# Performance work log

Hardware: AMD Instinct MI355X
Metric: run time of the kernel (lower is better)

The kernel has to match this reference:

```python
import jax, jax.numpy as jnp
import numpy as np

BLOCK = 16
MAX_LEVEL = 4
D = 256
W_INSIDE = 16.0  # CrossEntropyLoss weight for class 0
W_OUTSIDE = 1.0  # weight for class 1


def _blocks(gt, bs):
    # gt: [D,D,D] int -> [nb^3, bs, bs, bs] blocks in (x,y,z) order
    nb = gt.shape[0] // bs
    b = gt.reshape(nb, bs, nb, bs, nb, bs)
    return jnp.transpose(b, (0, 2, 4, 1, 3, 5)).reshape(nb ** 3, bs, bs, bs)


def setup_inputs() -> dict:
    key = jax.random.key(0)
    k1, k2, k3 = jax.random.split(key, 3)
    gt_label = jax.random.randint(k1, (1, D, D, D), 0, 2, dtype=jnp.int32)
    preds_full = jax.random.normal(k2, (4096, 2, BLOCK, BLOCK, BLOCK), dtype=jnp.float32)
    preds_single = jax.random.uniform(k3, (585, 3), dtype=jnp.float32)
    return {"gt_label": gt_label, "preds_full": preds_full, "preds_single": preds_single}


def reference(gt_label, preds_full, preds_single):
    gt = gt_label[0]  # [D,D,D]

    # ---- level 0: weighted cross-entropy per dense block (loss_fulls / loss_full_single) ----
    tgt = _blocks(gt, BLOCK)                              # [4096,16,16,16]
    logp = jax.nn.log_softmax(preds_full, axis=1)         # [4096,2,16,16,16]
    nll = -jnp.take_along_axis(logp, tgt[:, None].astype(jnp.int32), axis=1)[:, 0]
    w = jnp.where(tgt == 0, W_INSIDE, W_OUTSIDE)
    # torch weighted-mean CE: sum(w*nll)/sum(w) per block, then summed over blocks
    loss0 = jnp.sum(jnp.sum(w * nll, axis=(1, 2, 3)) / jnp.sum(w, axis=(1, 2, 3)))

    # ---- levels 1..MAX_LEVEL: ret += log(pred[0, gt]) per block (loss_singles) ----
    total = loss0
    offset = 0
    for level in range(1, MAX_LEVEL + 1):
        bs = BLOCK * 2 ** level
        nb = D // bs
        n = nb ** 3
        blk = _blocks(gt, bs).reshape(n, -1)
        mx = blk.max(axis=1)
        mn = blk.min(axis=1)
        g = jnp.where(mx != mn, 2, mx)                    # MIXED=2 or pure label
        p = preds_single[offset:offset + n]               # [n,3]
        total = total + jnp.sum(jnp.log(jnp.take_along_axis(p, g[:, None], axis=1)))
        offset += n
    return total
```

## Files before the change

kernel.cpp:

```cpp
#include <hip/hip_runtime.h>


#define W_INSIDE 16.0f

__global__ __launch_bounds__(256) void level0_kernel(
    const int* __restrict__ gt,
    const float* __restrict__ preds,
    unsigned char* __restrict__ flags,
    float* __restrict__ out)
{
    const int n  = blockIdx.x;
    const int bi = n >> 8, bj = (n >> 4) & 15, bk = n & 15;
    const int gbase = (bi * 16) * 65536 + (bj * 16) * 256 + (bk * 16);
    const float* __restrict__ p0 = preds + (size_t)n * 8192;
    const float* __restrict__ p1 = p0 + 4096;
    const int t = threadIdx.x;

    float wnll = 0.0f, wsum = 0.0f;
    int mn = 1, mx = 0;

    #pragma unroll
    for (int i = 0; i < 4; ++i) {
        const int v4 = t + 256 * i;
        const int x  = v4 >> 6;
        const int y  = (v4 >> 2) & 15;
        const int z4 = (v4 & 3) * 4;
        const int4   g4 = *reinterpret_cast<const int4*>(gt + gbase + x * 65536 + y * 256 + z4);
        const float4 a  = *reinterpret_cast<const float4*>(p0 + 4 * v4);
        const float4 b  = *reinterpret_cast<const float4*>(p1 + 4 * v4);

        const int   gs[4] = {g4.x, g4.y, g4.z, g4.w};
        const float av[4] = {a.x, a.y, a.z, a.w};
        const float bv[4] = {b.x, b.y, b.z, b.w};
        #pragma unroll
        for (int j = 0; j < 4; ++j) {
            const int tg = gs[j];
            mn = min(mn, tg);
            mx = max(mx, tg);
            const float d   = tg ? (bv[j] - av[j]) : (av[j] - bv[j]);
            const float nll = fmaxf(-d, 0.0f) + __logf(1.0f + __expf(-fabsf(d)));
            const float w   = tg ? 1.0f : W_INSIDE;
            wnll += w * nll;
            wsum += w;
        }
    }

    #pragma unroll
    for (int off = 32; off > 0; off >>= 1) {
        wnll += __shfl_down(wnll, off, 64);
        wsum += __shfl_down(wsum, off, 64);
        mn = min(mn, __shfl_down(mn, off, 64));
        mx = max(mx, __shfl_down(mx, off, 64));
    }
    __shared__ float s_wnll[4], s_wsum[4];
    __shared__ int   s_mn[4], s_mx[4];
    const int wave = t >> 6;
    if ((t & 63) == 0) { s_wnll[wave] = wnll; s_wsum[wave] = wsum; s_mn[wave] = mn; s_mx[wave] = mx; }
    __syncthreads();
    if (t == 0) {
        float W = 0.0f, S = 0.0f; int MN = 1, MX = 0;
        #pragma unroll
        for (int w = 0; w < 4; ++w) {
            W += s_wnll[w]; S += s_wsum[w];
            MN = min(MN, s_mn[w]); MX = max(MX, s_mx[w]);
        }
        atomicAdd(out, W / S);
        flags[n] = (unsigned char)(MN | (MX << 1));
    }
}

__global__ __launch_bounds__(512) void levels_kernel(
    const unsigned char* __restrict__ flags,
    const float* __restrict__ ps,
    float* __restrict__ out)
{
    __shared__ unsigned char s1[512];
    __shared__ unsigned char s2[64];
    __shared__ unsigned char s3[8];
    const int t = threadIdx.x;
    float acc = 0.0f;

    {
        const int bi = t >> 6, bj = (t >> 3) & 7, bk = t & 7;
        int mn = 1, mx = 0;
        #pragma unroll
        for (int di = 0; di < 2; ++di)
        #pragma unroll
        for (int dj = 0; dj < 2; ++dj)
        #pragma unroll
        for (int dk = 0; dk < 2; ++dk) {
            const unsigned char c = flags[(2*bi+di)*256 + (2*bj+dj)*16 + (2*bk+dk)];
            mn &= (c & 1);
            mx |= ((c >> 1) & 1);
        }
        const int g = (mn == mx) ? mx : 2;
        acc += __logf(ps[(0 + t) * 3 + g]);
        s1[t] = (unsigned char)(mn | (mx << 1));
    }
    __syncthreads();

    if (t < 64) {
        const int bi = t >> 4, bj = (t >> 2) & 3, bk = t & 3;
        int mn = 1, mx = 0;
        #pragma unroll
        for (int di = 0; di < 2; ++di)
        #pragma unroll
        for (int dj = 0; dj < 2; ++dj)
        #pragma unroll
        for (int dk = 0; dk < 2; ++dk) {
            const unsigned char c = s1[(2*bi+di)*64 + (2*bj+dj)*8 + (2*bk+dk)];
            mn &= (c & 1);
            mx |= ((c >> 1) & 1);
        }
        const int g = (mn == mx) ? mx : 2;
        acc += __logf(ps[(512 + t) * 3 + g]);
        s2[t] = (unsigned char)(mn | (mx << 1));
    }
    __syncthreads();

    if (t < 8) {
        const int bi = t >> 2, bj = (t >> 1) & 1, bk = t & 1;
        int mn = 1, mx = 0;
        #pragma unroll
        for (int di = 0; di < 2; ++di)
        #pragma unroll
        for (int dj = 0; dj < 2; ++dj)
        #pragma unroll
        for (int dk = 0; dk < 2; ++dk) {
            const unsigned char c = s2[(2*bi+di)*16 + (2*bj+dj)*4 + (2*bk+dk)];
            mn &= (c & 1);
            mx |= ((c >> 1) & 1);
        }
        const int g = (mn == mx) ? mx : 2;
        acc += __logf(ps[(576 + t) * 3 + g]);
        s3[t] = (unsigned char)(mn | (mx << 1));
    }
    __syncthreads();

    if (t == 0) {
        int mn = 1, mx = 0;
        #pragma unroll
        for (int c8 = 0; c8 < 8; ++c8) {
            mn &= (s3[c8] & 1);
            mx |= ((s3[c8] >> 1) & 1);
        }
        const int g = (mn == mx) ? mx : 2;
        acc += __logf(ps[584 * 3 + g]);
    }

    #pragma unroll
    for (int off = 32; off > 0; off >>= 1)
        acc += __shfl_down(acc, off, 64);
    __shared__ float s_acc[8];
    const int wave = t >> 6;
    if ((t & 63) == 0) s_acc[wave] = acc;
    __syncthreads();
    if (t == 0) {
        float S = 0.0f;
        #pragma unroll
        for (int w = 0; w < 8; ++w) S += s_acc[w];
        atomicAdd(out, S);
    }
}

extern "C" void kernel_launch(void* const* d_in, const int* in_sizes, int n_in,
                              void* d_out, int out_size, void* d_ws, size_t ws_size,
                              hipStream_t stream) {
    const int*   gt    = (const int*)d_in[0];
    const float* preds = (const float*)d_in[1];
    const float* ps    = (const float*)d_in[2];
    float* out = (float*)d_out;
    unsigned char* flags = (unsigned char*)d_ws;

    hipMemsetAsync(d_out, 0, out_size * sizeof(float), stream);
    level0_kernel<<<4096, 256, 0, stream>>>(gt, preds, flags, out);
    levels_kernel<<<1, 512, 0, stream>>>(flags, ps, out);
}
```

Before: 249.1 us.

## Pre-pack labels into per-block bitmasks and drop atomics and memset

Adds a pass that streams the int32 label volume once and packs it into 16-bit masks laid out per 16^3 block, so the level-0 kernel reads a compact mask instead of strided int4 label loads. Level-0 now issues all prediction loads up front with nontemporal hints and writes per-block losses to a buffer instead of using atomics. The final single-block kernel sums those losses and writes the output directly, which removes the memset. The cost is an extra kernel launch and an extra round trip of the label data, though the mask it writes back is small.

New measurement: 229.5 us. -7.9%, faster.

```diff
diff --git a/kernel.cpp b/kernel.cpp
--- a/kernel.cpp
+++ b/kernel.cpp
@@ -3,73 +3,111 @@
 
 #define W_INSIDE 16.0f
 
-__global__ __launch_bounds__(256) void level0_kernel(
+typedef int   vint4   __attribute__((ext_vector_type(4)));
+typedef float vfloat4 __attribute__((ext_vector_type(4)));
+
+__global__ __launch_bounds__(256) void gt_pack_kernel(
     const int* __restrict__ gt,
+    unsigned short* __restrict__ mask)
+{
+    const int T = blockIdx.x * 256 + threadIdx.x;
+    const vint4* p = reinterpret_cast<const vint4*>(gt) + 4 * (size_t)T;
+    const vint4 q0 = __builtin_nontemporal_load(p + 0);
+    const vint4 q1 = __builtin_nontemporal_load(p + 1);
+    const vint4 q2 = __builtin_nontemporal_load(p + 2);
+    const vint4 q3 = __builtin_nontemporal_load(p + 3);
+
+    unsigned m = 0;
+    m |= (q0.x & 1)        | ((q0.y & 1) << 1)  | ((q0.z & 1) << 2)  | ((q0.w & 1) << 3);
+    m |= ((q1.x & 1) << 4) | ((q1.y & 1) << 5)  | ((q1.z & 1) << 6)  | ((q1.w & 1) << 7);
+    m |= ((q2.x & 1) << 8) | ((q2.y & 1) << 9)  | ((q2.z & 1) << 10) | ((q2.w & 1) << 11);
+    m |= ((q3.x & 1) << 12)| ((q3.y & 1) << 13) | ((q3.z & 1) << 14) | ((q3.w & 1) << 15);
+
+    const int x = T >> 12, y = (T >> 4) & 255, z16 = T & 15;
+    const int n = ((x >> 4) << 8) | ((y >> 4) << 4) | z16;
+    mask[n * 256 + (x & 15) * 16 + (y & 15)] = (unsigned short)m;
+}
+
+__global__ __launch_bounds__(256, 4) void level0_kernel(
     const float* __restrict__ preds,
-    unsigned char* __restrict__ flags,
-    float* __restrict__ out)
+    const unsigned short* __restrict__ mask,
+    float* __restrict__ loss,
+    unsigned char* __restrict__ flags)
 {
-    const int n  = blockIdx.x;
-    const int bi = n >> 8, bj = (n >> 4) & 15, bk = n & 15;
-    const int gbase = (bi * 16) * 65536 + (bj * 16) * 256 + (bk * 16);
-    const float* __restrict__ p0 = preds + (size_t)n * 8192;
-    const float* __restrict__ p1 = p0 + 4096;
+    const int n = blockIdx.x;
     const int t = threadIdx.x;
+    const vfloat4* __restrict__ p0 = reinterpret_cast<const vfloat4*>(preds + (size_t)n * 8192);
+    const vfloat4* __restrict__ p1 = p0 + 1024;
+
+    const vfloat4 a0 = __builtin_nontemporal_load(p0 + t);
+    const vfloat4 a1 = __builtin_nontemporal_load(p0 + t + 256);
+    const vfloat4 a2 = __builtin_nontemporal_load(p0 + t + 512);
+    const vfloat4 a3 = __builtin_nontemporal_load(p0 + t + 768);
+    const vfloat4 b0 = __builtin_nontemporal_load(p1 + t);
+    const vfloat4 b1 = __builtin_nontemporal_load(p1 + t + 256);
+    const vfloat4 b2 = __builtin_nontemporal_load(p1 + t + 512);
+    const vfloat4 b3 = __builtin_nontemporal_load(p1 + t + 768);
+    __builtin_amdgcn_sched_barrier(0);
+
+    __shared__ unsigned short smask[256];
+    if (t < 32)
+        reinterpret_cast<vint4*>(smask)[t] =
+            *(reinterpret_cast<const vint4*>(mask + (size_t)n * 256) + t);
+    __syncthreads();
 
     float wnll = 0.0f, wsum = 0.0f;
-    int mn = 1, mx = 0;
-
-    #pragma unroll
-    for (int i = 0; i < 4; ++i) {
-        const int v4 = t + 256 * i;
-        const int x  = v4 >> 6;
-        const int y  = (v4 >> 2) & 15;
-        const int z4 = (v4 & 3) * 4;
-        const int4   g4 = *reinterpret_cast<const int4*>(gt + gbase + x * 65536 + y * 256 + z4);
-        const float4 a  = *reinterpret_cast<const float4*>(p0 + 4 * v4);
-        const float4 b  = *reinterpret_cast<const float4*>(p1 + 4 * v4);
-
-        const int   gs[4] = {g4.x, g4.y, g4.z, g4.w};
-        const float av[4] = {a.x, a.y, a.z, a.w};
-        const float bv[4] = {b.x, b.y, b.z, b.w};
-        #pragma unroll
-        for (int j = 0; j < 4; ++j) {
-            const int tg = gs[j];
-            mn = min(mn, tg);
-            mx = max(mx, tg);
-            const float d   = tg ? (bv[j] - av[j]) : (av[j] - bv[j]);
-            const float nll = fmaxf(-d, 0.0f) + __logf(1.0f + __expf(-fabsf(d)));
-            const float w   = tg ? 1.0f : W_INSIDE;
-            wnll += w * nll;
-            wsum += w;
-        }
-    }
+    unsigned andb = 0xFu, orb = 0u;
+
+    #define DO4(V, A, B)                                                          \
+    {                                                                             \
+        const int x_ = (V) >> 6, y_ = ((V) >> 2) & 15, z4_ = (V) & 3;             \
+        const unsigned bits = ((unsigned)smask[x_ * 16 + y_] >> (z4_ * 4)) & 0xFu;\
+        andb &= bits; orb |= bits;                                                \
+        const float av[4] = {A.x, A.y, A.z, A.w};                                 \
+        const float bv[4] = {B.x, B.y, B.z, B.w};                                 \
+        _Pragma("unroll")                                                         \
+        for (int j = 0; j < 4; ++j) {                                             \
+            const int tg = (bits >> j) & 1;                                       \
+            const float d   = tg ? (bv[j] - av[j]) : (av[j] - bv[j]);             \
+            const float nll = fmaxf(-d, 0.0f) + __logf(1.0f + __expf(-fabsf(d))); \
+            wnll += tg ? nll : W_INSIDE * nll;                                    \
+            wsum += tg ? 1.0f : W_INSIDE;                                         \
+        }                                                                         \
+    }
+    DO4(t,       a0, b0)
+    DO4(t + 256, a1, b1)
+    DO4(t + 512, a2, b2)
+    DO4(t + 768, a3, b3)
+    #undef DO4
 
     #pragma unroll
     for (int off = 32; off > 0; off >>= 1) {
         wnll += __shfl_down(wnll, off, 64);
         wsum += __shfl_down(wsum, off, 64);
-        mn = min(mn, __shfl_down(mn, off, 64));
-        mx = max(mx, __shfl_down(mx, off, 64));
+        andb &= (unsigned)__shfl_down((int)andb, off, 64);
+        orb  |= (unsigned)__shfl_down((int)orb,  off, 64);
     }
     __shared__ float s_wnll[4], s_wsum[4];
-    __shared__ int   s_mn[4], s_mx[4];
+    __shared__ unsigned s_and[4], s_or[4];
     const int wave = t >> 6;
-    if ((t & 63) == 0) { s_wnll[wave] = wnll; s_wsum[wave] = wsum; s_mn[wave] = mn; s_mx[wave] = mx; }
+    if ((t & 63) == 0) { s_wnll[wave] = wnll; s_wsum[wave] = wsum; s_and[wave] = andb; s_or[wave] = orb; }
     __syncthreads();
     if (t == 0) {
-        float W = 0.0f, S = 0.0f; int MN = 1, MX = 0;
+        float W = 0.0f, S = 0.0f; unsigned A_ = 0xFu, O_ = 0u;
         #pragma unroll
         for (int w = 0; w < 4; ++w) {
             W += s_wnll[w]; S += s_wsum[w];
-            MN = min(MN, s_mn[w]); MX = max(MX, s_mx[w]);
-        }
-        atomicAdd(out, W / S);
-        flags[n] = (unsigned char)(MN | (MX << 1));
+            A_ &= s_and[w]; O_ |= s_or[w];
+        }
+        loss[n]  = W / S;
+        const int mn = (A_ == 0xFu) ? 1 : 0;
+        const int mx = O_ ? 1 : 0;
+        flags[n] = (unsigned char)(mn | (mx << 1));
     }
 }
 
 __global__ __launch_bounds__(512) void levels_kernel(
+    const float* __restrict__ loss,
     const unsigned char* __restrict__ flags,
     const float* __restrict__ ps,
     float* __restrict__ out)
@@ -81,6 +119,12 @@
     float acc = 0.0f;
 
     {
+        const vfloat4 l0 = *(reinterpret_cast<const vfloat4*>(loss) + 2 * t);
+        const vfloat4 l1 = *(reinterpret_cast<const vfloat4*>(loss) + 2 * t + 1);
+        acc += (l0.x + l0.y) + (l0.z + l0.w) + (l1.x + l1.y) + (l1.z + l1.w);
+    }
+
+    {
         const int bi = t >> 6, bj = (t >> 3) & 7, bk = t & 7;
         int mn = 1, mx = 0;
         #pragma unroll
@@ -159,7 +203,7 @@
         float S = 0.0f;
         #pragma unroll
         for (int w = 0; w < 8; ++w) S += s_acc[w];
-        atomicAdd(out, S);
+        out[0] = S;
     }
 }
 
@@ -170,9 +214,12 @@
     const float* preds = (const float*)d_in[1];
     const float* ps    = (const float*)d_in[2];
     float* out = (float*)d_out;
-    unsigned char* flags = (unsigned char*)d_ws;
-
-    hipMemsetAsync(d_out, 0, out_size * sizeof(float), stream);
-    level0_kernel<<<4096, 256, 0, stream>>>(gt, preds, flags, out);
-    levels_kernel<<<1, 512, 0, stream>>>(flags, ps, out);
-}
+
+    unsigned short* maskbuf = (unsigned short*)d_ws;
+    float*          loss    = (float*)((char*)d_ws + (1 << 21));
+    unsigned char*  flagbuf = (unsigned char*)d_ws + (1 << 21) + 16384;
+
+    gt_pack_kernel<<<4096, 256, 0, stream>>>(gt, maskbuf);
+    level0_kernel<<<4096, 256, 0, stream>>>(preds, maskbuf, loss, flagbuf);
+    levels_kernel<<<1, 512, 0, stream>>>(loss, flagbuf, ps, out);
+}
```

## Process four z-adjacent blocks per workgroup with double-buffered loads and packed labels

Applied to the files above, without the earlier changes.

Each workgroup now handles four consecutive z blocks (1024 workgroups instead of 4096). Labels are loaded once as fully coalesced 64-byte rows, packed into 4-bit nibbles in shared memory, and the prediction loads are double-buffered against the compute. Weight sums come from popcounts of the packed labels. Per-block losses go to a workspace buffer that the second kernel sums, which removes the memset and the global atomics. The changes add register pressure, shared-memory traffic and scheduling barriers, and use nontemporal loads.

Result: faster. 218.5 us (-12.3%).

```diff
diff --git a/kernel.cpp b/kernel.cpp
--- a/kernel.cpp
+++ b/kernel.cpp
@@ -3,73 +3,106 @@
 
 #define W_INSIDE 16.0f
 
-__global__ __launch_bounds__(256) void level0_kernel(
+typedef int   vint4   __attribute__((ext_vector_type(4)));
+typedef float vfloat4 __attribute__((ext_vector_type(4)));
+
+__global__ __launch_bounds__(256, 2) void main_kernel(
     const int* __restrict__ gt,
     const float* __restrict__ preds,
-    unsigned char* __restrict__ flags,
-    float* __restrict__ out)
+    float* __restrict__ loss,
+    unsigned char* __restrict__ flags)
 {
-    const int n  = blockIdx.x;
-    const int bi = n >> 8, bj = (n >> 4) & 15, bk = n & 15;
-    const int gbase = (bi * 16) * 65536 + (bj * 16) * 256 + (bk * 16);
-    const float* __restrict__ p0 = preds + (size_t)n * 8192;
-    const float* __restrict__ p1 = p0 + 4096;
+    const int w = blockIdx.x;
     const int t = threadIdx.x;
-
-    float wnll = 0.0f, wsum = 0.0f;
-    int mn = 1, mx = 0;
-
-    #pragma unroll
-    for (int i = 0; i < 4; ++i) {
-        const int v4 = t + 256 * i;
-        const int x  = v4 >> 6;
-        const int y  = (v4 >> 2) & 15;
-        const int z4 = (v4 & 3) * 4;
-        const int4   g4 = *reinterpret_cast<const int4*>(gt + gbase + x * 65536 + y * 256 + z4);
-        const float4 a  = *reinterpret_cast<const float4*>(p0 + 4 * v4);
-        const float4 b  = *reinterpret_cast<const float4*>(p1 + 4 * v4);
-
-        const int   gs[4] = {g4.x, g4.y, g4.z, g4.w};
-        const float av[4] = {a.x, a.y, a.z, a.w};
-        const float bv[4] = {b.x, b.y, b.z, b.w};
-        #pragma unroll
-        for (int j = 0; j < 4; ++j) {
-            const int tg = gs[j];
-            mn = min(mn, tg);
-            mx = max(mx, tg);
-            const float d   = tg ? (bv[j] - av[j]) : (av[j] - bv[j]);
-            const float nll = fmaxf(-d, 0.0f) + __logf(1.0f + __expf(-fabsf(d)));
-            const float w   = tg ? 1.0f : W_INSIDE;
-            wnll += w * nll;
-            wsum += w;
-        }
-    }
-
-    #pragma unroll
-    for (int off = 32; off > 0; off >>= 1) {
-        wnll += __shfl_down(wnll, off, 64);
-        wsum += __shfl_down(wsum, off, 64);
-        mn = min(mn, __shfl_down(mn, off, 64));
-        mx = max(mx, __shfl_down(mx, off, 64));
-    }
-    __shared__ float s_wnll[4], s_wsum[4];
-    __shared__ int   s_mn[4], s_mx[4];
+    const int bi = w >> 6, bj = (w >> 2) & 15, q = w & 3;
+    const int n0 = bi * 256 + bj * 16 + 4 * q;
+
+    const vint4* __restrict__ gt4 = reinterpret_cast<const vint4*>(gt);
+    const int gbase = bi * 262144 + bj * 1024 + (t >> 4) * 64 + 16 * q + (t & 15);
+    vint4 G[16];
+    #pragma unroll
+    for (int i = 0; i < 16; ++i)
+        G[i] = __builtin_nontemporal_load(gt4 + gbase + i * 16384);
+
+    const vfloat4* __restrict__ pb = reinterpret_cast<const vfloat4*>(preds) + (size_t)n0 * 2048;
+    vfloat4 A[8], B[8];
+    #define LOAD8(DST, kk)                                                         \
+    {                                                                              \
+        _Pragma("unroll")                                                          \
+        for (int j = 0; j < 4; ++j) {                                              \
+            DST[j]     = __builtin_nontemporal_load(pb + (kk) * 2048 + t + 256 * j);          \
+            DST[4 + j] = __builtin_nontemporal_load(pb + (kk) * 2048 + 1024 + t + 256 * j);   \
+        }                                                                          \
+    }
+    LOAD8(A, 0)
+    __builtin_amdgcn_sched_barrier(0);
+
+    __shared__ unsigned char nib[4096];
+    #pragma unroll
+    for (int i = 0; i < 16; ++i) {
+        const unsigned m = (G[i].x & 1) | ((G[i].y & 1) << 1)
+                         | ((G[i].z & 1) << 2) | ((G[i].w & 1) << 3);
+        nib[i * 256 + t] = (unsigned char)m;
+    }
+    __syncthreads();
+
+    float wnll[4];
+    int   c1[4];
+
+    #define COMP(SRC, kk)                                                          \
+    {                                                                              \
+        float wn = 0.0f; int cc = 0;                                               \
+        _Pragma("unroll")                                                          \
+        for (int j = 0; j < 4; ++j) {                                              \
+            const int g = t + 256 * j;                                             \
+            const unsigned bits =                                                  \
+                nib[(g >> 6) * 256 + ((g >> 2) & 15) * 16 + (kk) * 4 + (g & 3)];   \
+            cc += __builtin_popcount(bits);                                        \
+            const float av[4] = {SRC[j].x, SRC[j].y, SRC[j].z, SRC[j].w};          \
+            const float bv[4] = {SRC[4+j].x, SRC[4+j].y, SRC[4+j].z, SRC[4+j].w};  \
+            _Pragma("unroll")                                                      \
+            for (int j2 = 0; j2 < 4; ++j2) {                                       \
+                const int tg = (bits >> j2) & 1;                                   \
+                const float d   = tg ? (bv[j2] - av[j2]) : (av[j2] - bv[j2]);      \
+                const float nll = fmaxf(-d, 0.0f) + __logf(1.0f + __expf(-fabsf(d))); \
+                wn += tg ? nll : W_INSIDE * nll;                                   \
+            }                                                                      \
+        }                                                                          \
+        wnll[kk] = wn; c1[kk] = cc;                                                \
+    }
+
+    LOAD8(B, 1) __builtin_amdgcn_sched_barrier(0); COMP(A, 0)
+    LOAD8(A, 2) __builtin_amdgcn_sched_barrier(0); COMP(B, 1)
+    LOAD8(B, 3) __builtin_amdgcn_sched_barrier(0); COMP(A, 2)
+    COMP(B, 3)
+    #undef LOAD8
+    #undef COMP
+
+    __shared__ float s_w[4][4];
+    __shared__ int   s_c[4][4];
     const int wave = t >> 6;
-    if ((t & 63) == 0) { s_wnll[wave] = wnll; s_wsum[wave] = wsum; s_mn[wave] = mn; s_mx[wave] = mx; }
-    __syncthreads();
-    if (t == 0) {
-        float W = 0.0f, S = 0.0f; int MN = 1, MX = 0;
-        #pragma unroll
-        for (int w = 0; w < 4; ++w) {
-            W += s_wnll[w]; S += s_wsum[w];
-            MN = min(MN, s_mn[w]); MX = max(MX, s_mx[w]);
-        }
-        atomicAdd(out, W / S);
-        flags[n] = (unsigned char)(MN | (MX << 1));
+    #pragma unroll
+    for (int k = 0; k < 4; ++k) {
+        float wv = wnll[k];
+        int   cv = c1[k];
+        #pragma unroll
+        for (int off = 32; off > 0; off >>= 1) {
+            wv += __shfl_down(wv, off, 64);
+            cv += __shfl_down(cv, off, 64);
+        }
+        if ((t & 63) == 0) { s_w[k][wave] = wv; s_c[k][wave] = cv; }
+    }
+    __syncthreads();
+    if (t < 4) {
+        const float W = (s_w[t][0] + s_w[t][1]) + (s_w[t][2] + s_w[t][3]);
+        const int   C = (s_c[t][0] + s_c[t][1]) + (s_c[t][2] + s_c[t][3]);
+        loss[n0 + t]  = W / (65536.0f - 15.0f * (float)C);
+        flags[n0 + t] = (unsigned char)((C == 4096 ? 1 : 0) | (C > 0 ? 2 : 0));
     }
 }
 
 __global__ __launch_bounds__(512) void levels_kernel(
+    const float* __restrict__ loss,
     const unsigned char* __restrict__ flags,
     const float* __restrict__ ps,
     float* __restrict__ out)
@@ -81,6 +114,12 @@
     float acc = 0.0f;
 
     {
+        const vfloat4 l0 = *(reinterpret_cast<const vfloat4*>(loss) + 2 * t);
+        const vfloat4 l1 = *(reinterpret_cast<const vfloat4*>(loss) + 2 * t + 1);
+        acc += (l0.x + l0.y) + (l0.z + l0.w) + (l1.x + l1.y) + (l1.z + l1.w);
+    }
+
+    {
         const int bi = t >> 6, bj = (t >> 3) & 7, bk = t & 7;
         int mn = 1, mx = 0;
         #pragma unroll
@@ -158,8 +197,8 @@
     if (t == 0) {
         float S = 0.0f;
         #pragma unroll
-        for (int w = 0; w < 8; ++w) S += s_acc[w];
-        atomicAdd(out, S);
+        for (int w8 = 0; w8 < 8; ++w8) S += s_acc[w8];
+        out[0] = S;
     }
 }
 
@@ -170,9 +209,10 @@
     const float* preds = (const float*)d_in[1];
     const float* ps    = (const float*)d_in[2];
     float* out = (float*)d_out;
-    unsigned char* flags = (unsigned char*)d_ws;
-
-    hipMemsetAsync(d_out, 0, out_size * sizeof(float), stream);
-    level0_kernel<<<4096, 256, 0, stream>>>(gt, preds, flags, out);
-    levels_kernel<<<1, 512, 0, stream>>>(flags, ps, out);
+
+    float*         loss    = (float*)d_ws;
+    unsigned char* flagbuf = (unsigned char*)d_ws + 16384;
+
+    main_kernel<<<1024, 256, 0, stream>>>(gt, preds, loss, flagbuf);
+    levels_kernel<<<1, 512, 0, stream>>>(loss, flagbuf, ps, out);
 }
```
